# Optimization experiments

Measured on AMD Instinct MI355X. Metric: run time of the kernel, lower is better.

The kernel has to match this reference:

```python
import jax, jax.numpy as jnp
import numpy as np

B, N, F_DIM = 32, 1024, 128
ALPHA = 0.2        # LeakyReLU negative slope
PAD = -9e15        # pad_sequence padding value in the original
DENSITY = 0.05


def setup_inputs() -> dict:
    key = jax.random.key(0)
    k1, k2, k3 = jax.random.split(key, 3)
    # sparse 0/1 adjacency with self-loops so every node has degree >= 1
    adj = (jax.random.uniform(k1, (B, N, N)) < DENSITY).astype(jnp.float32)
    eye = jnp.eye(N, dtype=jnp.float32)[None, :, :]
    adj = jnp.maximum(adj, eye)
    feats = jax.random.normal(k2, (B, N, F_DIM), dtype=jnp.float32)
    # xavier_uniform with leaky_relu gain on a [2F, 1]
    gain = float(np.sqrt(2.0 / (1.0 + ALPHA ** 2)))
    bound = gain * float(np.sqrt(6.0 / (2 * F_DIM + 1)))
    a = jax.random.uniform(k3, (2 * F_DIM, 1), minval=-bound, maxval=bound,
                           dtype=jnp.float32)
    return {"batch_graphs": adj, "batch_features": feats, "a": a}


def reference(batch_graphs, batch_features, a):
    # e_ij = LeakyReLU([h_i || h_j] @ a) decomposes as (h_i @ a1) + (h_j @ a2)
    s_src = batch_features @ a[:F_DIM, 0]   # [B, N] contribution of node i
    s_dst = batch_features @ a[F_DIM:, 0]   # [B, N] contribution of neighbor j
    e = s_src[:, :, None] + s_dst[:, None, :]            # [B, N, N]
    e = jnp.where(e >= 0, e, ALPHA * e)                   # LeakyReLU
    mask = batch_graphs == 1
    e = jnp.where(mask, e, PAD)                           # pad non-edges like pad_sequence
    att = jax.nn.softmax(e, axis=-1)                      # segmented softmax over neighbors
    att = jnp.where(mask, att, 0.0)                       # scatter back only real edges
    return att
```

## Files before the change

kernel.cpp:

```cpp
#include <hip/hip_runtime.h>
#include <hip/hip_bf16.h>
#include <stdint.h>

#define B_DIM 32
#define N_DIM 1024
#define F_DIM 128
#define ALPHA 0.2f
#define NROWS (B_DIM * N_DIM)
#define TAIL_ROWS 128
#define MAIN_ROWS (NROWS - TAIL_ROWS)
#define SCORE_BYTES ((size_t)(2 * NROWS) * sizeof(float))

typedef float          vf4 __attribute__((ext_vector_type(4)));
typedef unsigned short vh4 __attribute__((ext_vector_type(4)));

__device__ __forceinline__ unsigned short f32_to_bf16_bits(float f) {
    union { __hip_bfloat16 h; unsigned short u; } cvt;
    cvt.h = __float2bfloat16(f);
    return cvt.u;
}

__device__ __forceinline__ bool probe_is_f32(const void* adj) {
    return *(const uint32_t*)adj == 0x3F800000u;
}

template <bool F32>
__device__ __forceinline__ float* score_base(void* out) {
    const size_t out_bytes = (size_t)NROWS * N_DIM * (F32 ? 4 : 2);
    return (float*)((char*)out + out_bytes - SCORE_BYTES);
}

template <bool F32>
__device__ __forceinline__ void scores_body(
    const void* __restrict__ feats_v, const void* __restrict__ a_v, void* out)
{
    float* base  = score_base<F32>(out);
    float* s_src = base;
    float* s_dst = base + NROWS;

    const int wid  = threadIdx.x >> 6;
    const int lane = threadIdx.x & 63;
    const int pr   = blockIdx.x * 4 + wid;
    const int row  = pr * 2 + (lane >> 5);
    const int f0   = (lane & 31) * 4;

    float x0, x1, x2, x3, w10, w11, w12, w13, w20, w21, w22, w23;
    if (F32) {
        const vf4 xv  = *(const vf4*)((const float*)feats_v + (size_t)row * F_DIM + f0);
        const vf4 w1v = *(const vf4*)((const float*)a_v + f0);
        const vf4 w2v = *(const vf4*)((const float*)a_v + F_DIM + f0);
        x0 = xv.x;  x1 = xv.y;  x2 = xv.z;  x3 = xv.w;
        w10 = w1v.x; w11 = w1v.y; w12 = w1v.z; w13 = w1v.w;
        w20 = w2v.x; w21 = w2v.y; w22 = w2v.z; w23 = w2v.w;
    } else {
        const vh4 xv  = *(const vh4*)((const __hip_bfloat16*)feats_v + (size_t)row * F_DIM + f0);
        const vh4 w1v = *(const vh4*)((const __hip_bfloat16*)a_v + f0);
        const vh4 w2v = *(const vh4*)((const __hip_bfloat16*)a_v + F_DIM + f0);
        x0 = __uint_as_float((unsigned)xv.x << 16);  x1 = __uint_as_float((unsigned)xv.y << 16);
        x2 = __uint_as_float((unsigned)xv.z << 16);  x3 = __uint_as_float((unsigned)xv.w << 16);
        w10 = __uint_as_float((unsigned)w1v.x << 16); w11 = __uint_as_float((unsigned)w1v.y << 16);
        w12 = __uint_as_float((unsigned)w1v.z << 16); w13 = __uint_as_float((unsigned)w1v.w << 16);
        w20 = __uint_as_float((unsigned)w2v.x << 16); w21 = __uint_as_float((unsigned)w2v.y << 16);
        w22 = __uint_as_float((unsigned)w2v.z << 16); w23 = __uint_as_float((unsigned)w2v.w << 16);
    }

    float v1 = x0 * w10 + x1 * w11 + x2 * w12 + x3 * w13;
    float v2 = x0 * w20 + x1 * w21 + x2 * w22 + x3 * w23;
    #pragma unroll
    for (int off = 1; off < 32; off <<= 1) {
        v1 += __shfl_xor(v1, off, 64);
        v2 += __shfl_xor(v2, off, 64);
    }
    if ((lane & 31) == 0) { s_src[row] = v1; s_dst[row] = v2; }
}

__global__ __launch_bounds__(256) void scores_kernel(
    const void* __restrict__ adj, const void* __restrict__ feats,
    const void* __restrict__ a, void* out)
{
    if (probe_is_f32(adj)) scores_body<true>(feats, a, out);
    else                   scores_body<false>(feats, a, out);
}

__device__ __forceinline__ float qget(const vf4& q, int k) { return q[k]; }
__device__ __forceinline__ float qget(const vh4& q, int k) {
    return __uint_as_float((unsigned)q[k] << 16);
}

template <bool F32> struct QSel  { using T = vf4; };
template <>         struct QSel<false> { using T = vh4; };

template <bool F32>
__device__ __forceinline__ const typename QSel<F32>::T* adj_row(
    const void* __restrict__ adj_v, int row)
{
    if constexpr (F32)
        return (const vf4*)((const float*)adj_v + (size_t)row * N_DIM);
    else
        return (const vh4*)((const __hip_bfloat16*)adj_v + (size_t)row * N_DIM);
}

template <bool F32, class QV>
__device__ __forceinline__ void process_row4(
    void* __restrict__ out_v, int row, int lane, float ssrc,
    vf4 sd0, vf4 sd1, vf4 sd2, vf4 sd3,
    QV q0, QV q1, QV q2, QV q3)
{
    float lsum = 0.0f;
    {
        auto acc = [&](const vf4& sdv, const QV& qv) {
            #pragma unroll
            for (int k = 0; k < 4; ++k) {
                float t = ssrc + sdv[k];
                t = fmaxf(t, ALPHA * t);
                lsum += __expf(t) * qget(qv, k);
            }
        };
        acc(sd0, q0); acc(sd1, q1); acc(sd2, q2); acc(sd3, q3);
    }
    #pragma unroll
    for (int off = 1; off < 64; off <<= 1)
        lsum += __shfl_xor(lsum, off, 64);
    const float inv = 1.0f / lsum;

    {
        auto emit = [&](int c, const vf4& sdv, const QV& qv) {
            const int idx = c * 64 + lane;
            if constexpr (F32) {
                vf4 o;
                #pragma unroll
                for (int k = 0; k < 4; ++k) {
                    float t = ssrc + sdv[k];
                    t = fmaxf(t, ALPHA * t);
                    o[k] = __expf(t) * qget(qv, k) * inv;
                }
                ((vf4*)((float*)out_v + (size_t)row * N_DIM))[idx] = o;
            } else {
                vh4 o;
                #pragma unroll
                for (int k = 0; k < 4; ++k) {
                    float t = ssrc + sdv[k];
                    t = fmaxf(t, ALPHA * t);
                    o[k] = f32_to_bf16_bits(__expf(t) * qget(qv, k) * inv);
                }
                ((vh4*)((__hip_bfloat16*)out_v + (size_t)row * N_DIM))[idx] = o;
            }
        };
        emit(0, sd0, q0); emit(1, sd1, q1); emit(2, sd2, q2); emit(3, sd3, q3);
    }
}

template <bool F32>
__device__ __forceinline__ void main_body(const void* __restrict__ adj_v, void* out_v)
{
    using QV = typename QSel<F32>::T;

    const int wid  = threadIdx.x >> 6;
    const int lane = threadIdx.x & 63;
    const int gw   = blockIdx.x * 4 + wid;
    const int r0   = gw * 4;
    const int b    = r0 >> 10;

    const QV* A0 = adj_row<F32>(adj_v, r0);
    const QV* A1 = adj_row<F32>(adj_v, r0 + 1);
    QV a0 = A0[lane], a1 = A0[64 + lane], a2 = A0[128 + lane], a3 = A0[192 + lane];
    QV b0 = A1[lane], b1 = A1[64 + lane], b2 = A1[128 + lane], b3 = A1[192 + lane];
    __builtin_amdgcn_sched_barrier(0);

    const float* base = score_base<F32>(out_v);
    const float s0 = base[r0], s1 = base[r0 + 1], s2 = base[r0 + 2], s3 = base[r0 + 3];
    const vf4* SD = (const vf4*)(base + NROWS + (size_t)b * N_DIM);
    vf4 sd0 = SD[lane], sd1 = SD[64 + lane], sd2 = SD[128 + lane], sd3 = SD[192 + lane];

    process_row4<F32>(out_v, r0, lane, s0, sd0, sd1, sd2, sd3, a0, a1, a2, a3);

    const QV* A2 = adj_row<F32>(adj_v, r0 + 2);
    a0 = A2[lane]; a1 = A2[64 + lane]; a2 = A2[128 + lane]; a3 = A2[192 + lane];
    __builtin_amdgcn_sched_barrier(0);
    process_row4<F32>(out_v, r0 + 1, lane, s1, sd0, sd1, sd2, sd3, b0, b1, b2, b3);

    const QV* A3 = adj_row<F32>(adj_v, r0 + 3);
    b0 = A3[lane]; b1 = A3[64 + lane]; b2 = A3[128 + lane]; b3 = A3[192 + lane];
    __builtin_amdgcn_sched_barrier(0);
    process_row4<F32>(out_v, r0 + 2, lane, s2, sd0, sd1, sd2, sd3, a0, a1, a2, a3);

    process_row4<F32>(out_v, r0 + 3, lane, s3, sd0, sd1, sd2, sd3, b0, b1, b2, b3);
}

__global__ __launch_bounds__(256, 6) void main_kernel(
    const void* __restrict__ adj, void* out)
{
    if (probe_is_f32(adj)) main_body<true>(adj, out);
    else                   main_body<false>(adj, out);
}

template <bool F32>
__device__ __forceinline__ void tail_body(
    const void* __restrict__ adj_v, const void* __restrict__ feats_v,
    const void* __restrict__ a_v, void* __restrict__ out_v)
{
    __shared__ float sdst_sh[N_DIM];

    const int tid  = threadIdx.x;
    const int wid  = tid >> 6;
    const int lane = tid & 63;
    const int b    = B_DIM - 1;
    const int row  = MAIN_ROWS + blockIdx.x * 4 + wid;

    #pragma unroll
    for (int k = 0; k < 4; ++k) {
        const int j = tid * 4 + k;
        float acc = 0.0f;
        if (F32) {
            const vf4* fp = (const vf4*)((const float*)feats_v + ((size_t)b * N_DIM + j) * F_DIM);
            const vf4* ap = (const vf4*)((const float*)a_v + F_DIM);
            #pragma unroll 8
            for (int f = 0; f < F_DIM / 4; ++f) {
                const vf4 x = fp[f], w = ap[f];
                acc += x.x * w.x + x.y * w.y + x.z * w.z + x.w * w.w;
            }
        } else {
            const __hip_bfloat16* fp = (const __hip_bfloat16*)feats_v + ((size_t)b * N_DIM + j) * F_DIM;
            const __hip_bfloat16* ap = (const __hip_bfloat16*)a_v + F_DIM;
            #pragma unroll 8
            for (int f = 0; f < F_DIM; ++f)
                acc += __bfloat162float(fp[f]) * __bfloat162float(ap[f]);
        }
        sdst_sh[j] = acc;
    }

    float ssrc;
    {
        const int f0 = lane * 2;
        float x0, x1, a0, a1;
        if (F32) {
            const float* fp = (const float*)feats_v + (size_t)row * F_DIM + f0;
            const float* ap = (const float*)a_v;
            x0 = fp[0]; x1 = fp[1]; a0 = ap[f0]; a1 = ap[f0 + 1];
        } else {
            const __hip_bfloat16* fp = (const __hip_bfloat16*)feats_v + (size_t)row * F_DIM + f0;
            const __hip_bfloat16* ap = (const __hip_bfloat16*)a_v;
            x0 = __bfloat162float(fp[0]); x1 = __bfloat162float(fp[1]);
            a0 = __bfloat162float(ap[f0]); a1 = __bfloat162float(ap[f0 + 1]);
        }
        float v = x0 * a0 + x1 * a1;
        #pragma unroll
        for (int off = 32; off > 0; off >>= 1)
            v += __shfl_down(v, off, 64);
        ssrc = __shfl(v, 0, 64);
    }
    __syncthreads();

    using QV = typename QSel<F32>::T;
    const QV* Q = adj_row<F32>(adj_v, row);
    QV q0 = Q[lane], q1 = Q[64 + lane], q2 = Q[128 + lane], q3 = Q[192 + lane];
    const vf4* SDS = (const vf4*)sdst_sh;
    vf4 sd0 = SDS[lane], sd1 = SDS[64 + lane], sd2 = SDS[128 + lane], sd3 = SDS[192 + lane];
    process_row4<F32>(out_v, row, lane, ssrc, sd0, sd1, sd2, sd3, q0, q1, q2, q3);
}

__global__ __launch_bounds__(256) void tail_kernel(
    const void* __restrict__ adj, const void* __restrict__ feats,
    const void* __restrict__ a, void* __restrict__ out)
{
    if (probe_is_f32(adj)) tail_body<true>(adj, feats, a, out);
    else                   tail_body<false>(adj, feats, a, out);
}

extern "C" void kernel_launch(void* const* d_in, const int* in_sizes, int n_in,
                              void* d_out, int out_size, void* d_ws, size_t ws_size,
                              hipStream_t stream) {
    const void* adj   = d_in[0];
    const void* feats = d_in[1];
    const void* a     = d_in[2];
    (void)d_ws; (void)ws_size;

    scores_kernel<<<NROWS / 8, 256, 0, stream>>>(adj, feats, a, d_out);
    main_kernel<<<MAIN_ROWS / 16, 256, 0, stream>>>(adj, d_out);
    tail_kernel<<<TAIL_ROWS / 4, 256, 0, stream>>>(adj, feats, a, d_out);
}
```

Measured before the change: 267.3 us.

## Stage adjacency rows through LDS with double-buffered async global_load_lds

The main kernel now loads adjacency rows straight into double-buffered shared memory with global_load_lds, prefetching the next row while the current one is processed. Each block handles 32 rows over 8 iterations, where before each wave handled 4 rows out of registers. The bf16 path gets a dedicated 8-wide vector routine. This aims to hide global load latency and cut register pressure, at the cost of a block barrier every iteration, lower occupancy and half as many blocks.

```diff
diff --git a/kernel.cpp b/kernel.cpp
--- a/kernel.cpp
+++ b/kernel.cpp
@@ -13,6 +13,7 @@
 
 typedef float          vf4 __attribute__((ext_vector_type(4)));
 typedef unsigned short vh4 __attribute__((ext_vector_type(4)));
+typedef unsigned short vh8 __attribute__((ext_vector_type(8)));
 
 __device__ __forceinline__ unsigned short f32_to_bf16_bits(float f) {
     union { __hip_bfloat16 h; unsigned short u; } cvt;
@@ -150,44 +151,102 @@
     }
 }
 
+__device__ __forceinline__ void process_row_b16(
+    void* __restrict__ out_v, int row, int lane, float ssrc,
+    vf4 sd00, vf4 sd01, vf4 sd10, vf4 sd11, vh8 r0, vh8 r1)
+{
+    float lsum = 0.0f;
+    {
+        auto acc8 = [&](const vf4& sa, const vf4& sb, const vh8& r) {
+            #pragma unroll
+            for (int k = 0; k < 8; ++k) {
+                const float sdv = (k < 4) ? sa[k] : sb[k - 4];
+                float t = ssrc + sdv;
+                t = fmaxf(t, ALPHA * t);
+                lsum += __expf(t) * __uint_as_float((unsigned)r[k] << 16);
+            }
+        };
+        acc8(sd00, sd01, r0); acc8(sd10, sd11, r1);
+    }
+    #pragma unroll
+    for (int off = 1; off < 64; off <<= 1)
+        lsum += __shfl_xor(lsum, off, 64);
+    const float inv = 1.0f / lsum;
+
+    {
+        auto emit8 = [&](int c, const vf4& sa, const vf4& sb, const vh8& r) {
+            vh8 o;
+            #pragma unroll
+            for (int k = 0; k < 8; ++k) {
+                const float sdv = (k < 4) ? sa[k] : sb[k - 4];
+                float t = ssrc + sdv;
+                t = fmaxf(t, ALPHA * t);
+                o[k] = f32_to_bf16_bits(__expf(t) * __uint_as_float((unsigned)r[k] << 16) * inv);
+            }
+            ((vh8*)((__hip_bfloat16*)out_v + (size_t)row * N_DIM))[c * 64 + lane] = o;
+        };
+        emit8(0, sd00, sd01, r0); emit8(1, sd10, sd11, r1);
+    }
+}
+
 template <bool F32>
 __device__ __forceinline__ void main_body(const void* __restrict__ adj_v, void* out_v)
 {
-    using QV = typename QSel<F32>::T;
+    constexpr int ROWB   = F32 ? 4096 : 2048;
+    constexpr int CHUNKS = F32 ? 4 : 2;
+    __shared__ __align__(16) unsigned char smem[2][4][4096];
 
     const int wid  = threadIdx.x >> 6;
     const int lane = threadIdx.x & 63;
-    const int gw   = blockIdx.x * 4 + wid;
-    const int r0   = gw * 4;
-    const int b    = r0 >> 10;
-
-    const QV* A0 = adj_row<F32>(adj_v, r0);
-    const QV* A1 = adj_row<F32>(adj_v, r0 + 1);
-    QV a0 = A0[lane], a1 = A0[64 + lane], a2 = A0[128 + lane], a3 = A0[192 + lane];
-    QV b0 = A1[lane], b1 = A1[64 + lane], b2 = A1[128 + lane], b3 = A1[192 + lane];
-    __builtin_amdgcn_sched_barrier(0);
+    const int row0 = blockIdx.x * 32;
+    const int b    = row0 >> 10;
 
     const float* base = score_base<F32>(out_v);
-    const float s0 = base[r0], s1 = base[r0 + 1], s2 = base[r0 + 2], s3 = base[r0 + 3];
-    const vf4* SD = (const vf4*)(base + NROWS + (size_t)b * N_DIM);
-    vf4 sd0 = SD[lane], sd1 = SD[64 + lane], sd2 = SD[128 + lane], sd3 = SD[192 + lane];
-
-    process_row4<F32>(out_v, r0, lane, s0, sd0, sd1, sd2, sd3, a0, a1, a2, a3);
-
-    const QV* A2 = adj_row<F32>(adj_v, r0 + 2);
-    a0 = A2[lane]; a1 = A2[64 + lane]; a2 = A2[128 + lane]; a3 = A2[192 + lane];
-    __builtin_amdgcn_sched_barrier(0);
-    process_row4<F32>(out_v, r0 + 1, lane, s1, sd0, sd1, sd2, sd3, b0, b1, b2, b3);
-
-    const QV* A3 = adj_row<F32>(adj_v, r0 + 3);
-    b0 = A3[lane]; b1 = A3[64 + lane]; b2 = A3[128 + lane]; b3 = A3[192 + lane];
-    __builtin_amdgcn_sched_barrier(0);
-    process_row4<F32>(out_v, r0 + 2, lane, s2, sd0, sd1, sd2, sd3, a0, a1, a2, a3);
-
-    process_row4<F32>(out_v, r0 + 3, lane, s3, sd0, sd1, sd2, sd3, b0, b1, b2, b3);
-}
-
-__global__ __launch_bounds__(256, 6) void main_kernel(
+    const vf4*   SD   = (const vf4*)(base + NROWS + (size_t)b * N_DIM);
+
+    vf4 sdA, sdB, sdC, sdD;
+    if constexpr (F32) {
+        sdA = SD[lane]; sdB = SD[64 + lane]; sdC = SD[128 + lane]; sdD = SD[192 + lane];
+    } else {
+        sdA = SD[2 * lane]; sdB = SD[2 * lane + 1];
+        sdC = SD[128 + 2 * lane]; sdD = SD[128 + 2 * lane + 1];
+    }
+
+    const char* adjc = (const char*)adj_v;
+    auto STAGE = [&](int t, int buf) {
+        const int row = row0 + t * 4 + wid;
+        const char* g = adjc + (size_t)row * ROWB + lane * 16;
+        #pragma unroll
+        for (int c = 0; c < CHUNKS; ++c)
+            __builtin_amdgcn_global_load_lds(
+                (const __attribute__((address_space(1))) unsigned int*)(g + c * 1024),
+                (__attribute__((address_space(3))) unsigned int*)(&smem[buf][wid][c * 1024]),
+                16, 0, 0);
+    };
+
+    STAGE(0, 0);
+    __syncthreads();
+    int cur = 0;
+    #pragma unroll 1
+    for (int t = 0; t < 8; ++t) {
+        if (t < 7) STAGE(t + 1, cur ^ 1);
+        const int   row  = row0 + t * 4 + wid;
+        const float ssrc = base[row];
+        if constexpr (F32) {
+            const vf4* Q = (const vf4*)(&smem[cur][wid][0]);
+            vf4 q0 = Q[lane], q1 = Q[64 + lane], q2 = Q[128 + lane], q3 = Q[192 + lane];
+            process_row4<true>(out_v, row, lane, ssrc, sdA, sdB, sdC, sdD, q0, q1, q2, q3);
+        } else {
+            const vh8* Q = (const vh8*)(&smem[cur][wid][0]);
+            vh8 r0 = Q[lane], r1 = Q[64 + lane];
+            process_row_b16(out_v, row, lane, ssrc, sdA, sdB, sdC, sdD, r0, r1);
+        }
+        __syncthreads();
+        cur ^= 1;
+    }
+}
+
+__global__ __launch_bounds__(256, 4) void main_kernel(
     const void* __restrict__ adj, void* out)
 {
     if (probe_is_f32(adj)) main_body<true>(adj, out);
@@ -276,6 +335,6 @@
     (void)d_ws; (void)ws_size;
 
     scores_kernel<<<NROWS / 8, 256, 0, stream>>>(adj, feats, a, d_out);
-    main_kernel<<<MAIN_ROWS / 16, 256, 0, stream>>>(adj, d_out);
+    main_kernel<<<MAIN_ROWS / 32, 256, 0, stream>>>(adj, d_out);
     tail_kernel<<<TAIL_ROWS / 4, 256, 0, stream>>>(adj, feats, a, d_out);
 }
```

Result: no change. 270.8 us (+1.3%).

## Split fused softmax into separate row-sum and emit kernels

Applied to the files above, without the earlier changes.

Replaces the single main kernel, which loaded each adjacency row once and computed both the exp-sum and the normalized output, with two kernels. The first computes per-row inverse sums into scratch space at the end of the output buffer. The second rereads the adjacency and writes the normalized output using one block per row. The tail region and the scratch area grow to hold the inverse sums. This doubles the adjacency reads in exchange for simpler, higher-parallelism kernels.

```diff
diff --git a/kernel.cpp b/kernel.cpp
--- a/kernel.cpp
+++ b/kernel.cpp
@@ -7,9 +7,9 @@
 #define F_DIM 128
 #define ALPHA 0.2f
 #define NROWS (B_DIM * N_DIM)
-#define TAIL_ROWS 128
+#define TAIL_ROWS 192
 #define MAIN_ROWS (NROWS - TAIL_ROWS)
-#define SCORE_BYTES ((size_t)(2 * NROWS) * sizeof(float))
+#define SCORE_BYTES ((size_t)(3 * NROWS) * sizeof(float))
 
 typedef float          vf4 __attribute__((ext_vector_type(4)));
 typedef unsigned short vh4 __attribute__((ext_vector_type(4)));
@@ -28,6 +28,24 @@
 __device__ __forceinline__ float* score_base(void* out) {
     const size_t out_bytes = (size_t)NROWS * N_DIM * (F32 ? 4 : 2);
     return (float*)((char*)out + out_bytes - SCORE_BYTES);
+}
+
+__device__ __forceinline__ float qget(const vf4& q, int k) { return q[k]; }
+__device__ __forceinline__ float qget(const vh4& q, int k) {
+    return __uint_as_float((unsigned)q[k] << 16);
+}
+
+template <bool F32> struct QSel  { using T = vf4; };
+template <>         struct QSel<false> { using T = vh4; };
+
+template <bool F32>
+__device__ __forceinline__ const typename QSel<F32>::T* adj_row(
+    const void* __restrict__ adj_v, int row)
+{
+    if constexpr (F32)
+        return (const vf4*)((const float*)adj_v + (size_t)row * N_DIM);
+    else
+        return (const vh4*)((const __hip_bfloat16*)adj_v + (size_t)row * N_DIM);
 }
 
 template <bool F32>
@@ -82,22 +100,114 @@
     else                   scores_body<false>(feats, a, out);
 }
 
-__device__ __forceinline__ float qget(const vf4& q, int k) { return q[k]; }
-__device__ __forceinline__ float qget(const vh4& q, int k) {
-    return __uint_as_float((unsigned)q[k] << 16);
-}
-
-template <bool F32> struct QSel  { using T = vf4; };
-template <>         struct QSel<false> { using T = vh4; };
-
-template <bool F32>
-__device__ __forceinline__ const typename QSel<F32>::T* adj_row(
-    const void* __restrict__ adj_v, int row)
-{
-    if constexpr (F32)
-        return (const vf4*)((const float*)adj_v + (size_t)row * N_DIM);
-    else
-        return (const vh4*)((const __hip_bfloat16*)adj_v + (size_t)row * N_DIM);
+template <bool F32>
+__device__ __forceinline__ void lsum_body(
+    const void* __restrict__ adj_v, void* __restrict__ out_v)
+{
+    using QV = typename QSel<F32>::T;
+    const int wid  = threadIdx.x >> 6;
+    const int lane = threadIdx.x & 63;
+    const int gw   = blockIdx.x * 4 + wid;
+    const int r0   = gw * 4;
+    const int b    = r0 >> 10;
+
+    float* base = score_base<F32>(out_v);
+    float* invp = base + 2 * NROWS;
+    const vf4* SD = (const vf4*)(base + NROWS + (size_t)b * N_DIM);
+
+    const float s0 = base[r0], s1 = base[r0 + 1], s2 = base[r0 + 2], s3 = base[r0 + 3];
+    const QV* A0 = adj_row<F32>(adj_v, r0);
+    const QV* A1 = adj_row<F32>(adj_v, r0 + 1);
+    const QV* A2 = adj_row<F32>(adj_v, r0 + 2);
+    const QV* A3 = adj_row<F32>(adj_v, r0 + 3);
+
+    float a0 = 0.0f, a1 = 0.0f, a2 = 0.0f, a3 = 0.0f;
+    #pragma unroll
+    for (int c = 0; c < 4; ++c) {
+        const int idx = c * 64 + lane;
+        const vf4 sd = SD[idx];
+        const QV q0 = A0[idx];
+        const QV q1 = A1[idx];
+        const QV q2 = A2[idx];
+        const QV q3 = A3[idx];
+        #pragma unroll
+        for (int k = 0; k < 4; ++k) {
+            float t0 = s0 + sd[k]; t0 = fmaxf(t0, ALPHA * t0);
+            float t1 = s1 + sd[k]; t1 = fmaxf(t1, ALPHA * t1);
+            float t2 = s2 + sd[k]; t2 = fmaxf(t2, ALPHA * t2);
+            float t3 = s3 + sd[k]; t3 = fmaxf(t3, ALPHA * t3);
+            a0 += __expf(t0) * qget(q0, k);
+            a1 += __expf(t1) * qget(q1, k);
+            a2 += __expf(t2) * qget(q2, k);
+            a3 += __expf(t3) * qget(q3, k);
+        }
+    }
+
+    #pragma unroll
+    for (int off = 1; off < 64; off <<= 1) {
+        a0 += __shfl_xor(a0, off, 64);
+        a1 += __shfl_xor(a1, off, 64);
+        a2 += __shfl_xor(a2, off, 64);
+        a3 += __shfl_xor(a3, off, 64);
+    }
+    if (lane == 0) {
+        invp[r0]     = 1.0f / a0;
+        invp[r0 + 1] = 1.0f / a1;
+        invp[r0 + 2] = 1.0f / a2;
+        invp[r0 + 3] = 1.0f / a3;
+    }
+}
+
+__global__ __launch_bounds__(256) void lsum_kernel(
+    const void* __restrict__ adj, void* out)
+{
+    if (probe_is_f32(adj)) lsum_body<true>(adj, out);
+    else                   lsum_body<false>(adj, out);
+}
+
+template <bool F32>
+__device__ __forceinline__ void emit_body(
+    const void* __restrict__ adj_v, void* __restrict__ out_v)
+{
+    using QV = typename QSel<F32>::T;
+    const int wid  = threadIdx.x >> 6;
+    const int lane = threadIdx.x & 63;
+    const int row  = blockIdx.x;
+    const int b    = row >> 10;
+    const int idx  = wid * 64 + lane;
+
+    const float* base = score_base<F32>(out_v);
+    const float ssrc = base[row];
+    const float inv  = (base + 2 * NROWS)[row];
+    const vf4 sd = ((const vf4*)(base + NROWS + (size_t)b * N_DIM))[idx];
+    const QV  q  = adj_row<F32>(adj_v, row)[idx];
+
+    if constexpr (F32) {
+        vf4 o;
+        #pragma unroll
+        for (int k = 0; k < 4; ++k) {
+            float t = ssrc + sd[k];
+            t = fmaxf(t, ALPHA * t);
+            o[k] = __expf(t) * qget(q, k) * inv;
+        }
+        ((vf4*)((float*)out_v + (size_t)row * N_DIM))[idx] = o;
+    } else {
+        vh4 o;
+        #pragma unroll
+        for (int k = 0; k < 4; ++k) {
+            float t = ssrc + sd[k];
+            t = fmaxf(t, ALPHA * t);
+            o[k] = f32_to_bf16_bits(__expf(t) * qget(q, k) * inv);
+        }
+        ((vh4*)((__hip_bfloat16*)out_v + (size_t)row * N_DIM))[idx] = o;
+    }
+}
+
+__global__ __launch_bounds__(256) void emit_kernel(
+    const void* __restrict__ adj, void* out)
+{
+    if (probe_is_f32(adj)) emit_body<true>(adj, out);
+    else                   emit_body<false>(adj, out);
 }
 
 template <bool F32, class QV>
@@ -151,50 +261,6 @@
 }
 
 template <bool F32>
-__device__ __forceinline__ void main_body(const void* __restrict__ adj_v, void* out_v)
-{
-    using QV = typename QSel<F32>::T;
-
-    const int wid  = threadIdx.x >> 6;
-    const int lane = threadIdx.x & 63;
-    const int gw   = blockIdx.x * 4 + wid;
-    const int r0   = gw * 4;
-    const int b    = r0 >> 10;
-
-    const QV* A0 = adj_row<F32>(adj_v, r0);
-    const QV* A1 = adj_row<F32>(adj_v, r0 + 1);
-    QV a0 = A0[lane], a1 = A0[64 + lane], a2 = A0[128 + lane], a3 = A0[192 + lane];
-    QV b0 = A1[lane], b1 = A1[64 + lane], b2 = A1[128 + lane], b3 = A1[192 + lane];
-    __builtin_amdgcn_sched_barrier(0);
-
-    const float* base = score_base<F32>(out_v);
-    const float s0 = base[r0], s1 = base[r0 + 1], s2 = base[r0 + 2], s3 = base[r0 + 3];
-    const vf4* SD = (const vf4*)(base + NROWS + (size_t)b * N_DIM);
-    vf4 sd0 = SD[lane], sd1 = SD[64 + lane], sd2 = SD[128 + lane], sd3 = SD[192 + lane];
-
-    process_row4<F32>(out_v, r0, lane, s0, sd0, sd1, sd2, sd3, a0, a1, a2, a3);
-
-    const QV* A2 = adj_row<F32>(adj_v, r0 + 2);
-    a0 = A2[lane]; a1 = A2[64 + lane]; a2 = A2[128 + lane]; a3 = A2[192 + lane];
-    __builtin_amdgcn_sched_barrier(0);
-    process_row4<F32>(out_v, r0 + 1, lane, s1, sd0, sd1, sd2, sd3, b0, b1, b2, b3);
-
-    const QV* A3 = adj_row<F32>(adj_v, r0 + 3);
-    b0 = A3[lane]; b1 = A3[64 + lane]; b2 = A3[128 + lane]; b3 = A3[192 + lane];
-    __builtin_amdgcn_sched_barrier(0);
-    process_row4<F32>(out_v, r0 + 2, lane, s2, sd0, sd1, sd2, sd3, a0, a1, a2, a3);
-
-    process_row4<F32>(out_v, r0 + 3, lane, s3, sd0, sd1, sd2, sd3, b0, b1, b2, b3);
-}
-
-__global__ __launch_bounds__(256, 6) void main_kernel(
-    const void* __restrict__ adj, void* out)
-{
-    if (probe_is_f32(adj)) main_body<true>(adj, out);
-    else                   main_body<false>(adj, out);
-}
-
-template <bool F32>
 __device__ __forceinline__ void tail_body(
     const void* __restrict__ adj_v, const void* __restrict__ feats_v,
     const void* __restrict__ a_v, void* __restrict__ out_v)
@@ -276,6 +342,7 @@
     (void)d_ws; (void)ws_size;
 
     scores_kernel<<<NROWS / 8, 256, 0, stream>>>(adj, feats, a, d_out);
-    main_kernel<<<MAIN_ROWS / 16, 256, 0, stream>>>(adj, d_out);
+    lsum_kernel<<<NROWS / 16, 256, 0, stream>>>(adj, d_out);
+    emit_kernel<<<MAIN_ROWS, 256, 0, stream>>>(adj, d_out);
     tail_kernel<<<TAIL_ROWS / 4, 256, 0, stream>>>(adj, feats, a, d_out);
 }
```

Measured after the change: 279.6 us. 1.05x slower.

## Split fused softmax into row-sum pass and grid-stride emit pass

Applied to the files above, without the earlier changes.

Replaces the fused main kernel, where each wave handled four rows and computed the sum and the output together, with two kernels. The first computes each row's reciprocal exp-sum into an extra scratch region at the end of the output buffer. The second is a flat grid-stride kernel that streams adjacency in 16-byte chunks and writes the normalized output. This aims for better occupancy and wider vector access, but it reads the adjacency matrix twice and adds a kernel launch. The tail row count grows to fit the larger scratch region.

```diff
diff --git a/kernel.cpp b/kernel.cpp
--- a/kernel.cpp
+++ b/kernel.cpp
@@ -7,12 +7,14 @@
 #define F_DIM 128
 #define ALPHA 0.2f
 #define NROWS (B_DIM * N_DIM)
-#define TAIL_ROWS 128
+#define TAIL_ROWS 192
 #define MAIN_ROWS (NROWS - TAIL_ROWS)
-#define SCORE_BYTES ((size_t)(2 * NROWS) * sizeof(float))
+#define SCORE_BYTES ((size_t)(3 * NROWS) * sizeof(float))
+#define EMIT_THREADS (2048 * 256)
 
 typedef float          vf4 __attribute__((ext_vector_type(4)));
 typedef unsigned short vh4 __attribute__((ext_vector_type(4)));
+typedef unsigned short vh8 __attribute__((ext_vector_type(8)));
 
 __device__ __forceinline__ unsigned short f32_to_bf16_bits(float f) {
     union { __hip_bfloat16 h; unsigned short u; } cvt;
@@ -29,6 +31,11 @@
     const size_t out_bytes = (size_t)NROWS * N_DIM * (F32 ? 4 : 2);
     return (float*)((char*)out + out_bytes - SCORE_BYTES);
 }
+
+__device__ __forceinline__ float bf2f(unsigned short u) {
+    return __uint_as_float((unsigned)u << 16);
+}
+__device__ __forceinline__ float leaky(float t) { return fmaxf(t, ALPHA * t); }
 
 template <bool F32>
 __device__ __forceinline__ void scores_body(
@@ -56,12 +63,9 @@
         const vh4 xv  = *(const vh4*)((const __hip_bfloat16*)feats_v + (size_t)row * F_DIM + f0);
         const vh4 w1v = *(const vh4*)((const __hip_bfloat16*)a_v + f0);
         const vh4 w2v = *(const vh4*)((const __hip_bfloat16*)a_v + F_DIM + f0);
-        x0 = __uint_as_float((unsigned)xv.x << 16);  x1 = __uint_as_float((unsigned)xv.y << 16);
-        x2 = __uint_as_float((unsigned)xv.z << 16);  x3 = __uint_as_float((unsigned)xv.w << 16);
-        w10 = __uint_as_float((unsigned)w1v.x << 16); w11 = __uint_as_float((unsigned)w1v.y << 16);
-        w12 = __uint_as_float((unsigned)w1v.z << 16); w13 = __uint_as_float((unsigned)w1v.w << 16);
-        w20 = __uint_as_float((unsigned)w2v.x << 16); w21 = __uint_as_float((unsigned)w2v.y << 16);
-        w22 = __uint_as_float((unsigned)w2v.z << 16); w23 = __uint_as_float((unsigned)w2v.w << 16);
+        x0 = bf2f(xv.x);  x1 = bf2f(xv.y);  x2 = bf2f(xv.z);  x3 = bf2f(xv.w);
+        w10 = bf2f(w1v.x); w11 = bf2f(w1v.y); w12 = bf2f(w1v.z); w13 = bf2f(w1v.w);
+        w20 = bf2f(w2v.x); w21 = bf2f(w2v.y); w22 = bf2f(w2v.z); w23 = bf2f(w2v.w);
     }
 
     float v1 = x0 * w10 + x1 * w11 + x2 * w12 + x3 * w13;
@@ -82,10 +86,127 @@
     else                   scores_body<false>(feats, a, out);
 }
 
+template <bool F32>
+__device__ __forceinline__ void lsum_body(
+    const void* __restrict__ adj_v, void* __restrict__ out_v)
+{
+    const int wid  = threadIdx.x >> 6;
+    const int lane = threadIdx.x & 63;
+    const int row  = blockIdx.x * 4 + wid;
+    const int b    = row >> 10;
+
+    float* base = score_base<F32>(out_v);
+    float* invp = base + 2 * NROWS;
+    const float ssrc = base[row];
+
+    float pa = 0.0f, pb = 0.0f, pc = 0.0f, pd = 0.0f;
+
+    if constexpr (F32) {
+        const vf4* A  = (const vf4*)((const float*)adj_v + (size_t)row * N_DIM);
+        const vf4* SD = (const vf4*)(base + NROWS + (size_t)b * N_DIM);
+        vf4 q0 = A[lane], q1 = A[64 + lane], q2 = A[128 + lane], q3 = A[192 + lane];
+        vf4 s0 = SD[lane], s1 = SD[64 + lane], s2 = SD[128 + lane], s3 = SD[192 + lane];
+        __builtin_amdgcn_sched_barrier(0);
+        #pragma unroll
+        for (int k = 0; k < 4; ++k) {
+            pa += __expf(leaky(ssrc + s0[k])) * q0[k];
+            pb += __expf(leaky(ssrc + s1[k])) * q1[k];
+            pc += __expf(leaky(ssrc + s2[k])) * q2[k];
+            pd += __expf(leaky(ssrc + s3[k])) * q3[k];
+        }
+    } else {
+        const vh8* A  = (const vh8*)((const __hip_bfloat16*)adj_v + (size_t)row * N_DIM);
+        const vf4* SD = (const vf4*)(base + NROWS + (size_t)b * N_DIM);
+        vh8 r0 = A[lane], r1 = A[64 + lane];
+        vf4 s00 = SD[2 * lane], s01 = SD[2 * lane + 1];
+        vf4 s10 = SD[128 + 2 * lane], s11 = SD[128 + 2 * lane + 1];
+        __builtin_amdgcn_sched_barrier(0);
+        #pragma unroll
+        for (int k = 0; k < 4; ++k) {
+            pa += __expf(leaky(ssrc + s00[k])) * bf2f(r0[k]);
+            pb += __expf(leaky(ssrc + s01[k])) * bf2f(r0[k + 4]);
+            pc += __expf(leaky(ssrc + s10[k])) * bf2f(r1[k]);
+            pd += __expf(leaky(ssrc + s11[k])) * bf2f(r1[k + 4]);
+        }
+    }
+
+    float lsum = (pa + pb) + (pc + pd);
+    #pragma unroll
+    for (int off = 1; off < 64; off <<= 1)
+        lsum += __shfl_xor(lsum, off, 64);
+    if (lane == 0) invp[row] = 1.0f / lsum;
+}
+
+__global__ __launch_bounds__(256) void lsum_kernel(
+    const void* __restrict__ adj, void* out)
+{
+    if (probe_is_f32(adj)) lsum_body<true>(adj, out);
+    else                   lsum_body<false>(adj, out);
+}
+
+template <bool F32>
+__device__ __forceinline__ void emit_body(
+    const void* __restrict__ adj_v, void* __restrict__ out_v)
+{
+    const int g = blockIdx.x * 256 + threadIdx.x;
+    const float* base = score_base<F32>(out_v);
+    const float* invp = base + 2 * NROWS;
+    const float* sdst = base + NROWS;
+
+    if constexpr (F32) {
+        const int CH = MAIN_ROWS * (N_DIM / 4);
+        const vf4* A = (const vf4*)adj_v;
+        vf4*       O = (vf4*)out_v;
+        #pragma unroll 1
+        for (int j = g; j < CH; j += EMIT_THREADS) {
+            const int row = j >> 8;
+            const int b   = row >> 10;
+            const int c   = j & 255;
+            const vf4 q  = A[j];
+            const vf4 sd = ((const vf4*)(sdst + (size_t)b * N_DIM))[c];
+            const float ssrc = base[row];
+            const float inv  = invp[row];
+            vf4 o;
+            #pragma unroll
+            for (int k = 0; k < 4; ++k)
+                o[k] = __expf(leaky(ssrc + sd[k])) * q[k] * inv;
+            O[j] = o;
+        }
+    } else {
+        const int CH = MAIN_ROWS * (N_DIM / 8);
+        const vh8* A = (const vh8*)adj_v;
+        vh8*       O = (vh8*)out_v;
+        #pragma unroll 1
+        for (int j = g; j < CH; j += EMIT_THREADS) {
+            const int row = j >> 7;
+            const int b   = row >> 10;
+            const int c   = j & 127;
+            const vh8 r  = A[j];
+            const vf4 sa = ((const vf4*)(sdst + (size_t)b * N_DIM))[c * 2];
+            const vf4 sb = ((const vf4*)(sdst + (size_t)b * N_DIM))[c * 2 + 1];
+            const float ssrc = base[row];
+            const float inv  = invp[row];
+            vh8 o;
+            #pragma unroll
+            for (int k = 0; k < 4; ++k)
+                o[k] = f32_to_bf16_bits(__expf(leaky(ssrc + sa[k])) * bf2f(r[k]) * inv);
+            #pragma unroll
+            for (int k = 0; k < 4; ++k)
+                o[k + 4] = f32_to_bf16_bits(__expf(leaky(ssrc + sb[k])) * bf2f(r[k + 4]) * inv);
+            O[j] = o;
+        }
+    }
+}
+
+__global__ __launch_bounds__(256) void emit_kernel(
+    const void* __restrict__ adj, void* out)
+{
+    if (probe_is_f32(adj)) emit_body<true>(adj, out);
+    else                   emit_body<false>(adj, out);
+}
+
 __device__ __forceinline__ float qget(const vf4& q, int k) { return q[k]; }
-__device__ __forceinline__ float qget(const vh4& q, int k) {
-    return __uint_as_float((unsigned)q[k] << 16);
-}
+__device__ __forceinline__ float qget(const vh4& q, int k) { return bf2f(q[k]); }
 
 template <bool F32> struct QSel  { using T = vf4; };
 template <>         struct QSel<false> { using T = vh4; };
@@ -110,11 +231,8 @@
     {
         auto acc = [&](const vf4& sdv, const QV& qv) {
             #pragma unroll
-            for (int k = 0; k < 4; ++k) {
-                float t = ssrc + sdv[k];
-                t = fmaxf(t, ALPHA * t);
-                lsum += __expf(t) * qget(qv, k);
-            }
+            for (int k = 0; k < 4; ++k)
+                lsum += __expf(leaky(ssrc + sdv[k])) * qget(qv, k);
         };
         acc(sd0, q0); acc(sd1, q1); acc(sd2, q2); acc(sd3, q3);
     }
@@ -129,69 +247,19 @@
             if constexpr (F32) {
                 vf4 o;
                 #pragma unroll
-                for (int k = 0; k < 4; ++k) {
-                    float t = ssrc + sdv[k];
-                    t = fmaxf(t, ALPHA * t);
-                    o[k] = __expf(t) * qget(qv, k) * inv;
-                }
+                for (int k = 0; k < 4; ++k)
+                    o[k] = __expf(leaky(ssrc + sdv[k])) * qget(qv, k) * inv;
                 ((vf4*)((float*)out_v + (size_t)row * N_DIM))[idx] = o;
             } else {
                 vh4 o;
                 #pragma unroll
-                for (int k = 0; k < 4; ++k) {
-                    float t = ssrc + sdv[k];
-                    t = fmaxf(t, ALPHA * t);
-                    o[k] = f32_to_bf16_bits(__expf(t) * qget(qv, k) * inv);
-                }
+                for (int k = 0; k < 4; ++k)
+                    o[k] = f32_to_bf16_bits(__expf(leaky(ssrc + sdv[k])) * qget(qv, k) * inv);
                 ((vh4*)((__hip_bfloat16*)out_v + (size_t)row * N_DIM))[idx] = o;
             }
         };
         emit(0, sd0, q0); emit(1, sd1, q1); emit(2, sd2, q2); emit(3, sd3, q3);
     }
-}
-
-template <bool F32>
-__device__ __forceinline__ void main_body(const void* __restrict__ adj_v, void* out_v)
-{
-    using QV = typename QSel<F32>::T;
-
-    const int wid  = threadIdx.x >> 6;
-    const int lane = threadIdx.x & 63;
-    const int gw   = blockIdx.x * 4 + wid;
-    const int r0   = gw * 4;
-    const int b    = r0 >> 10;
-
-    const QV* A0 = adj_row<F32>(adj_v, r0);
-    const QV* A1 = adj_row<F32>(adj_v, r0 + 1);
-    QV a0 = A0[lane], a1 = A0[64 + lane], a2 = A0[128 + lane], a3 = A0[192 + lane];
-    QV b0 = A1[lane], b1 = A1[64 + lane], b2 = A1[128 + lane], b3 = A1[192 + lane];
-    __builtin_amdgcn_sched_barrier(0);
-
-    const float* base = score_base<F32>(out_v);
-    const float s0 = base[r0], s1 = base[r0 + 1], s2 = base[r0 + 2], s3 = base[r0 + 3];
-    const vf4* SD = (const vf4*)(base + NROWS + (size_t)b * N_DIM);
-    vf4 sd0 = SD[lane], sd1 = SD[64 + lane], sd2 = SD[128 + lane], sd3 = SD[192 + lane];
-
-    process_row4<F32>(out_v, r0, lane, s0, sd0, sd1, sd2, sd3, a0, a1, a2, a3);
-
-    const QV* A2 = adj_row<F32>(adj_v, r0 + 2);
-    a0 = A2[lane]; a1 = A2[64 + lane]; a2 = A2[128 + lane]; a3 = A2[192 + lane];
-    __builtin_amdgcn_sched_barrier(0);
-    process_row4<F32>(out_v, r0 + 1, lane, s1, sd0, sd1, sd2, sd3, b0, b1, b2, b3);
-
-    const QV* A3 = adj_row<F32>(adj_v, r0 + 3);
-    b0 = A3[lane]; b1 = A3[64 + lane]; b2 = A3[128 + lane]; b3 = A3[192 + lane];
-    __builtin_amdgcn_sched_barrier(0);
-    process_row4<F32>(out_v, r0 + 2, lane, s2, sd0, sd1, sd2, sd3, a0, a1, a2, a3);
-
-    process_row4<F32>(out_v, r0 + 3, lane, s3, sd0, sd1, sd2, sd3, b0, b1, b2, b3);
-}
-
-__global__ __launch_bounds__(256, 6) void main_kernel(
-    const void* __restrict__ adj, void* out)
-{
-    if (probe_is_f32(adj)) main_body<true>(adj, out);
-    else                   main_body<false>(adj, out);
 }
 
 template <bool F32>
@@ -276,6 +344,7 @@
     (void)d_ws; (void)ws_size;
 
     scores_kernel<<<NROWS / 8, 256, 0, stream>>>(adj, feats, a, d_out);
-    main_kernel<<<MAIN_ROWS / 16, 256, 0, stream>>>(adj, d_out);
+    lsum_kernel<<<NROWS / 4, 256, 0, stream>>>(adj, d_out);
+    emit_kernel<<<2048, 256, 0, stream>>>(adj, d_out);
     tail_kernel<<<TAIL_ROWS / 4, 256, 0, stream>>>(adj, feats, a, d_out);
 }
```

Result: slower. 277.3 us (+3.7%).
